# Performance work log

Hardware: AMD Instinct MI355X
Metric: run time of the kernel (lower is better)

The kernel has to match this reference:

```python
import math
import jax
import jax.numpy as jnp
import numpy as np

GRID = 12  # distance + 1 for distance-11 surface code


def _ln(x, s, b):
    m = jnp.mean(x, axis=-1, keepdims=True)
    v = jnp.mean((x - m) ** 2, axis=-1, keepdims=True)
    return (x - m) / jnp.sqrt(v + 1e-5) * s + b


def _gelu(x):
    return jax.nn.gelu(x, approximate=False)  # torch F.gelu default = exact erf


def _forward(meas, event, leak, event_leak, bias, pm_w, pm_b, pe_w, pe_b, pl_w, pl_b, pel_w, pel_b,
             stab_emb, cyc_emb, er_ln_s, er_ln_b, er_fc1_w, er_fc1_b, er_fc2_w, er_fc2_b,
             ln1_s, ln1_b, Wb, Wq, bq, Wk, bk, Wv, bv, Wo, bo, ln2_s, ln2_b,
             f1_w, f1_b, f2_w, f2_b, conv_w, conv_b, lnf_s, lnf_b,
             P, sc_w, sc_b, dr_w, dr_b, rb1_w, rb1_b, rb2_w, rb2_b, out_w, out_b,
             stab_ids, cycle_ids):
    B, T, S = meas.shape
    L, Hh, _, da = Wq.shape
    dm = Wv.shape[-1]
    d = P.shape[0]

    # per-head additive attention bias, identical across cycles: (L,B,H,S,S)
    Bp = jnp.einsum('bijd,ldh->lbhij', bias, Wb)
    scale = 1.0 / jnp.sqrt(jnp.asarray(da, meas.dtype))
    pos_emb = stab_emb[stab_ids]  # (S, d)

    def embed(t):
        h = (meas[:, t, :, None] * pm_w + pm_b
             + event[:, t, :, None] * pe_w + pe_b
             + leak[:, t, :, None] * pl_w + pl_b
             + event_leak[:, t, :, None] * pel_w + pel_b
             + pos_emb[None] + cyc_emb[cycle_ids[t]][None, None, :])
        for r in range(er_fc1_w.shape[0]):
            hn = _ln(h, er_ln_s[r], er_ln_b[r])
            h = h + jnp.matmul(_gelu(jnp.matmul(hn, er_fc1_w[r]) + er_fc1_b[r]), er_fc2_w[r]) + er_fc2_b[r]
        return h

    X = jnp.zeros((B, S, d), meas.dtype)
    for t in range(T):  # recurrent application of RNNCore over cycles
        X = (X + embed(t)) / jnp.sqrt(jnp.asarray(2.0, meas.dtype))
        for l in range(L):
            Xn = _ln(X, ln1_s[l], ln1_b[l])
            Q = jnp.einsum('bsd,hde->bhse', Xn, Wq[l]) + bq[l][None, :, None, :]
            Kt = jnp.einsum('bsd,hde->bhse', Xn, Wk[l]) + bk[l][None, :, None, :]
            V = jnp.einsum('bsd,hdm->bhsm', Xn, Wv[l]) + bv[l][None, :, None, :]
            Sc = jnp.einsum('bhqe,bhke->bhqk', Q, Kt) + Bp[l]  # bias added BEFORE 1/sqrt(da)
            A = jax.nn.softmax(Sc * scale, axis=-1)
            O = jnp.einsum('bhqk,bhkm->bhqm', A, V)
            Y = O.transpose(0, 2, 1, 3).reshape(B, S, Hh * dm)
            X = X + jnp.matmul(Y, Wo[l]) + bo[l]
            Xn = _ln(X, ln2_s[l], ln2_b[l])
            Yf = jnp.matmul(Xn, f1_w[l]) + f1_b[l]
            a, g = jnp.split(Yf, 2, axis=-1)
            X = X + jnp.matmul(_gelu(a) * g, f2_w[l]) + f2_b[l]
            # conv block: residual depth-mixing Conv1d(k=3, SAME) over the stabilizer axis
            xc = jnp.transpose(X, (0, 2, 1))  # (B, d, S)
            c = jax.lax.conv_general_dilated(xc, conv_w[l], (1,), 'SAME',
                                             dimension_numbers=('NCH', 'OIH', 'NCH'))
            X = X + _gelu(jnp.transpose(c + conv_b[l][None, :, None], (0, 2, 1)))

    # readout
    Xn = _ln(X, lnf_s, lnf_b)
    pad = jnp.broadcast_to(P, (B, GRID * GRID - S, d))  # empty grid cells filled with P
    grid = jnp.concatenate([Xn, pad], axis=1).reshape(B, GRID, GRID, d).transpose(0, 3, 1, 2)
    x = jax.lax.conv_general_dilated(grid, sc_w, (2, 2), 'VALID',
                                     dimension_numbers=('NCHW', 'OIHW', 'NCHW')) + sc_b[None, :, None, None]
    x = _gelu(x)
    x = jnp.einsum('bdhw,rd->brhw', x, dr_w) + dr_b[None, :, None, None]
    x = _gelu(x)
    x = x.mean(axis=2)  # basis 'z': pool over grid rows -> (B, rd, K)
    Kk = x.shape[2]
    x = x.transpose(0, 2, 1).reshape(B * Kk, -1)
    for r in range(rb1_w.shape[0]):
        x = x + jnp.matmul(_gelu(jnp.matmul(x, rb1_w[r]) + rb1_b[r]), rb2_w[r]) + rb2_b[r]
    logits = (jnp.matmul(x, out_w) + out_b).reshape(B, Kk).mean(axis=1)
    return logits


def setup_inputs() -> dict:
    key = jax.random.key(0)
    ks = iter(jax.random.split(key, 100))

    def rn(shape, s=0.02):
        return (s * jax.random.normal(next(ks), shape)).astype(jnp.float32)

    B, T, S, d = 16, 8, 120, 128
    L, H, da, dm, db = 2, 4, 32, 32, 32
    rd, nrb, ncyc = 48, 16, 32
    z = lambda *sh: jnp.zeros(sh, jnp.float32)
    o = lambda *sh: jnp.ones(sh, jnp.float32)
    inp = {
        'meas': jax.random.uniform(next(ks), (B, T, S), jnp.float32),
        'event': jax.random.uniform(next(ks), (B, T, S), jnp.float32),
        'leak': jax.random.uniform(next(ks), (B, T, S), jnp.float32),
        'event_leak': jax.random.uniform(next(ks), (B, T, S), jnp.float32),
        'bias': rn((B, S, S, db), 0.5),
        'pm_w': rn((d,)), 'pm_b': z(d),
        'pe_w': rn((d,)), 'pe_b': z(d),
        'pl_w': rn((d,)), 'pl_b': z(d),
        'pel_w': rn((d,)), 'pel_b': z(d),
        'stab_emb': rn((S, d)),
        'cyc_emb': rn((ncyc, d)),
        'er_ln_s': o(2, d), 'er_ln_b': z(2, d),
        'er_fc1_w': rn((2, d, d)), 'er_fc1_b': z(2, d),
        'er_fc2_w': rn((2, d, d)), 'er_fc2_b': z(2, d),
        'ln1_s': o(L, d), 'ln1_b': z(L, d),
        'Wb': rn((L, db, H)),
        'Wq': rn((L, H, d, da)), 'bq': z(L, H, da),
        'Wk': rn((L, H, d, da)), 'bk': z(L, H, da),
        'Wv': rn((L, H, d, dm)), 'bv': z(L, H, dm),
        'Wo': rn((L, H * dm, d)), 'bo': z(L, d),
        'ln2_s': o(L, d), 'ln2_b': z(L, d),
        'f1_w': rn((L, d, 4 * d)), 'f1_b': z(L, 4 * d),
        'f2_w': rn((L, 2 * d, d)), 'f2_b': z(L, d),
        'conv_w': rn((L, d, d, 3)), 'conv_b': z(L, d),
        'lnf_s': o(d), 'lnf_b': z(d),
        'P': z(d),
        'sc_w': rn((d, d, 2, 2)), 'sc_b': z(d),
        'dr_w': rn((rd, d)), 'dr_b': z(rd),
        'rb1_w': rn((nrb, rd, rd)), 'rb1_b': z(nrb, rd),
        'rb2_w': rn((nrb, rd, rd)), 'rb2_b': z(nrb, rd),
        'out_w': rn((rd,)), 'out_b': z(),
        'stab_ids': jnp.arange(S, dtype=jnp.int32),
        'cycle_ids': jnp.arange(T, dtype=jnp.int32),
    }
    return inp


def reference(meas, event, leak, event_leak, bias, pm_w, pm_b, pe_w, pe_b, pl_w, pl_b, pel_w, pel_b,
              stab_emb, cyc_emb, er_ln_s, er_ln_b, er_fc1_w, er_fc1_b, er_fc2_w, er_fc2_b,
              ln1_s, ln1_b, Wb, Wq, bq, Wk, bk, Wv, bv, Wo, bo, ln2_s, ln2_b,
              f1_w, f1_b, f2_w, f2_b, conv_w, conv_b, lnf_s, lnf_b,
              P, sc_w, sc_b, dr_w, dr_b, rb1_w, rb1_b, rb2_w, rb2_b, out_w, out_b,
              stab_ids, cycle_ids):
    return _forward(meas, event, leak, event_leak, bias, pm_w, pm_b, pe_w, pe_b, pl_w, pl_b, pel_w, pel_b,
                    stab_emb, cyc_emb, er_ln_s, er_ln_b, er_fc1_w, er_fc1_b, er_fc2_w, er_fc2_b,
                    ln1_s, ln1_b, Wb, Wq, bq, Wk, bk, Wv, bv, Wo, bo, ln2_s, ln2_b,
                    f1_w, f1_b, f2_w, f2_b, conv_w, conv_b, lnf_s, lnf_b,
                    P, sc_w, sc_b, dr_w, dr_b, rb1_w, rb1_b, rb2_w, rb2_b, out_w, out_b,
                    stab_ids, cycle_ids)
```

## Files before the change

kernel.cpp:

```cpp
#include <hip/hip_runtime.h>
#include <math.h>

#define Dm 128
#define Ssz 120
#define Bsz 16
#define Tcy 8
#define Hh 4
#define DA 32
#define Lly 2
#define RT 8
#define NRT ((Bsz*Ssz)/RT)
#define NROW (Bsz*Ssz)

struct KParams {
    const float *meas, *event_, *leak, *event_leak, *bias;
    const float *pm_w, *pm_b, *pe_w, *pe_b, *pl_w, *pl_b, *pel_w, *pel_b;
    const float *stab_emb, *cyc_emb;
    const float *er_ln_s, *er_ln_b, *er_fc1_w, *er_fc1_b, *er_fc2_w, *er_fc2_b;
    const float *ln1_s, *ln1_b, *Wb, *Wq, *bq, *Wk, *bk, *Wv, *bv, *Wo, *bo;
    const float *ln2_s, *ln2_b, *f1_w, *f1_b, *f2_w, *f2_b, *conv_w, *conv_b;
    const float *lnf_s, *lnf_b, *Pp, *sc_w, *sc_b, *dr_w, *dr_b;
    const float *rb1_w, *rb1_b, *rb2_w, *rb2_b, *out_w, *out_b;
    const int *stab_ids, *cycle_ids;
    float *Bp, *Q, *K, *V, *Y2, *cwT, *E;
};

__device__ __forceinline__ float gelu_f(float x) {
    return 0.5f * x * (1.0f + erff(x * 0.70710678118654752f));
}

__device__ __forceinline__ int swz16(int i, int per_b) {
    return ((((i & 7) << 1) | ((i >> 3) & 1)) * per_b) + (i >> 4);
}

__device__ __forceinline__ void ln_rows8(const float (*src)[Dm], float (*dst)[Dm],
                                         const float* sg, const float* bg, int tid) {
    int r = tid >> 6, g = tid & 63;
    float x0 = src[r][g], x1 = src[r][g + 64];
    float s1 = x0 + x1;
#pragma unroll
    for (int off = 32; off; off >>= 1) s1 += __shfl_xor(s1, off);
    float m = s1 * (1.f / 128.f);
    float d0 = x0 - m, d1 = x1 - m;
    float s2 = d0 * d0 + d1 * d1;
#pragma unroll
    for (int off = 32; off; off >>= 1) s2 += __shfl_xor(s2, off);
    float rstd = rsqrtf(s2 * (1.f / 128.f) + 1e-5f);
    dst[r][g]      = d0 * rstd * sg[g]      + bg[g];
    dst[r][g + 64] = d1 * rstd * sg[g + 64] + bg[g + 64];
}

__device__ __forceinline__ void ln32(const float (*src)[Dm], float (*dst)[Dm],
                                     const float* sg, const float* bg, int tid) {
    int r = tid >> 4, g = tid & 15;
    float v[8];
    float s1 = 0.f;
#pragma unroll
    for (int k = 0; k < 8; k++) { v[k] = src[r][g + 16 * k]; s1 += v[k]; }
#pragma unroll
    for (int off = 8; off; off >>= 1) s1 += __shfl_xor(s1, off);
    float m = s1 * (1.f / 128.f);
    float s2 = 0.f;
#pragma unroll
    for (int k = 0; k < 8; k++) { float d = v[k] - m; s2 += d * d; }
#pragma unroll
    for (int off = 8; off; off >>= 1) s2 += __shfl_xor(s2, off);
    float rstd = rsqrtf(s2 * (1.f / 128.f) + 1e-5f);
#pragma unroll
    for (int k = 0; k < 8; k++)
        dst[r][g + 16 * k] = (v[k] - m) * rstd * sg[g + 16 * k] + bg[g + 16 * k];
}

__global__ __launch_bounds__(256) void k_prepcw(KParams p) {
    int idx = blockIdx.x * 256 + threadIdx.x;
    if (idx >= Lly * Dm * 3 * Dm) return;
    int o = idx & 127; int rest = idx >> 7;
    int k = rest % 3; rest /= 3;
    int i = rest & 127; int l = rest >> 7;
    p.cwT[idx] = p.conv_w[((l * Dm + o) * Dm + i) * 3 + k];
}

__global__ __launch_bounds__(128) void k_bias(KParams p) {
    int blk = blockIdx.x;
    int b = blk / Ssz, i = blk % Ssz;
    int j = threadIdx.x;
    if (j >= Ssz) return;
    const float4* br4 = (const float4*)(p.bias + ((size_t)(b * Ssz + i) * Ssz + j) * 32);
    float a[Lly][4];
#pragma unroll
    for (int l = 0; l < Lly; l++)
#pragma unroll
        for (int h = 0; h < 4; h++) a[l][h] = 0.f;
#pragma unroll
    for (int c4 = 0; c4 < 8; c4++) {
        float bv[4]; *(float4*)bv = br4[c4];
#pragma unroll
        for (int u = 0; u < 4; u++) {
#pragma unroll
            for (int l = 0; l < Lly; l++) {
                const float* w = p.Wb + (l * 32 + c4 * 4 + u) * Hh;
                a[l][0] += bv[u] * w[0]; a[l][1] += bv[u] * w[1];
                a[l][2] += bv[u] * w[2]; a[l][3] += bv[u] * w[3];
            }
        }
    }
    size_t hs = (size_t)Ssz * Ssz;
#pragma unroll
    for (int l = 0; l < Lly; l++) {
        size_t base = (((size_t)(l * Bsz + b) * Hh) * Ssz + i) * Ssz + j;
        p.Bp[base] = a[l][0]; p.Bp[base + hs] = a[l][1];
        p.Bp[base + 2 * hs] = a[l][2]; p.Bp[base + 3 * hs] = a[l][3];
    }
}

__global__ __launch_bounds__(512) void k_embed_all(KParams p) {
    __shared__ float h[32][Dm], hn[32][Dm], t1[32][Dm];
    int t = blockIdx.x / 60, tile = blockIdx.x % 60;
    int row0 = tile * 32;
    int tid = threadIdx.x;
    int cid = p.cycle_ids[t];
    for (int idx = tid; idx < 32 * Dm; idx += 512) {
        int r = idx >> 7, j = idx & 127;
        int row = row0 + r;
        int b = row / Ssz, s = row % Ssz;
        int sid = p.stab_ids[s];
        int mi = (b * Tcy + t) * Ssz + s;
        h[r][j] = p.meas[mi] * p.pm_w[j] + p.pm_b[j]
                + p.event_[mi] * p.pe_w[j] + p.pe_b[j]
                + p.leak[mi] * p.pl_w[j] + p.pl_b[j]
                + p.event_leak[mi] * p.pel_w[j] + p.pel_b[j]
                + p.stab_emb[sid * Dm + j] + p.cyc_emb[cid * Dm + j];
    }
    __syncthreads();
    int g2 = tid >> 7, j = tid & 127;
    for (int rbk = 0; rbk < 2; rbk++) {
        ln32(h, hn, p.er_ln_s + rbk * Dm, p.er_ln_b + rbk * Dm, tid);
        __syncthreads();
        const float* W1 = p.er_fc1_w + rbk * Dm * Dm;
        float acc[8];
#pragma unroll
        for (int rr = 0; rr < 8; rr++) acc[rr] = 0.f;
#pragma unroll 2
        for (int i4 = 0; i4 < 32; i4++) {
            float4 xv[8];
#pragma unroll
            for (int rr = 0; rr < 8; rr++) xv[rr] = *(const float4*)&hn[8 * g2 + rr][i4 * 4];
#pragma unroll
            for (int u = 0; u < 4; u++) {
                float w = W1[(i4 * 4 + u) * Dm + j];
#pragma unroll
                for (int rr = 0; rr < 8; rr++) acc[rr] += ((const float*)&xv[rr])[u] * w;
            }
        }
        float b1 = p.er_fc1_b[rbk * Dm + j];
#pragma unroll
        for (int rr = 0; rr < 8; rr++) t1[8 * g2 + rr][j] = gelu_f(acc[rr] + b1);
        __syncthreads();
        const float* W2 = p.er_fc2_w + rbk * Dm * Dm;
#pragma unroll
        for (int rr = 0; rr < 8; rr++) acc[rr] = 0.f;
#pragma unroll 2
        for (int i4 = 0; i4 < 32; i4++) {
            float4 xv[8];
#pragma unroll
            for (int rr = 0; rr < 8; rr++) xv[rr] = *(const float4*)&t1[8 * g2 + rr][i4 * 4];
#pragma unroll
            for (int u = 0; u < 4; u++) {
                float w = W2[(i4 * 4 + u) * Dm + j];
#pragma unroll
                for (int rr = 0; rr < 8; rr++) acc[rr] += ((const float*)&xv[rr])[u] * w;
            }
        }
        float b2 = p.er_fc2_b[rbk * Dm + j];
#pragma unroll
        for (int rr = 0; rr < 8; rr++) h[8 * g2 + rr][j] += acc[rr] + b2;
        __syncthreads();
    }
    for (int idx = tid; idx < 32 * Dm; idx += 512) {
        int r = idx >> 7, jj = idx & 127;
        p.E[((size_t)t * NROW + row0 + r) * Dm + jj] = h[r][jj];
    }
}

__global__ __launch_bounds__(512) void k_a(KParams p, const float* Xprev, float* Xcur,
                                           int l, int t, int doConv) {
    __shared__ float xr[RT + 2][Dm];
    __shared__ float xn[RT][Dm];
    int rb = swz16(blockIdx.x, Ssz / RT);
    int row0 = rb * RT;
    int b = row0 / Ssz, s0 = row0 % Ssz;
    int tid = threadIdx.x;
    const float inv = 0.70710678118654752f;
    int g2 = tid >> 7, j = tid & 127;

    if (doConv) {
        int lconv = l ^ 1;
        {
            float4* xr4 = (float4*)&xr[0][0];
            for (int i = tid; i < (RT + 2) * Dm / 4; i += 512) {
                int rr = i >> 5, c = i & 31;
                int s = s0 + rr - 1;
                float4 v = make_float4(0.f, 0.f, 0.f, 0.f);
                if (s >= 0 && s < Ssz) v = *(const float4*)(Xprev + (b * Ssz + s) * Dm + 4 * c);
                xr4[i] = v;
            }
        }
        __syncthreads();
        const float* CW = p.cwT + (size_t)lconv * Dm * 3 * Dm + j;
        float a0 = 0.f, a1 = 0.f;
#pragma unroll 2
        for (int i4 = 0; i4 < 32; i4++) {
            float4 xv[4];
#pragma unroll
            for (int rr = 0; rr < 4; rr++) xv[rr] = *(const float4*)&xr[2 * g2 + rr][i4 * 4];
#pragma unroll
            for (int u = 0; u < 4; u++) {
                int i = i4 * 4 + u;
                float w0 = CW[(i * 3 + 0) * Dm];
                float w1 = CW[(i * 3 + 1) * Dm];
                float w2 = CW[(i * 3 + 2) * Dm];
                a0 += w0 * ((const float*)&xv[0])[u] + w1 * ((const float*)&xv[1])[u] + w2 * ((const float*)&xv[2])[u];
                a1 += w0 * ((const float*)&xv[1])[u] + w1 * ((const float*)&xv[2])[u] + w2 * ((const float*)&xv[3])[u];
            }
        }
        float cb = p.conv_b[lconv * Dm + j];
        float v0 = xr[2 * g2 + 1][j] + gelu_f(a0 + cb);
        float v1 = xr[2 * g2 + 2][j] + gelu_f(a1 + cb);
        if (l == 0) {
            v0 = (v0 + p.E[((size_t)t * NROW + row0 + 2 * g2) * Dm + j]) * inv;
            v1 = (v1 + p.E[((size_t)t * NROW + row0 + 2 * g2 + 1) * Dm + j]) * inv;
        }
        Xcur[(row0 + 2 * g2) * Dm + j]     = v0;
        Xcur[(row0 + 2 * g2 + 1) * Dm + j] = v1;
        xn[2 * g2][j] = v0; xn[2 * g2 + 1][j] = v1;
    } else {
        float v0 = p.E[(size_t)(row0 + 2 * g2) * Dm + j] * inv;
        float v1 = p.E[(size_t)(row0 + 2 * g2 + 1) * Dm + j] * inv;
        Xcur[(row0 + 2 * g2) * Dm + j]     = v0;
        Xcur[(row0 + 2 * g2 + 1) * Dm + j] = v1;
        xn[2 * g2][j] = v0; xn[2 * g2 + 1][j] = v1;
    }
    __syncthreads();
    ln_rows8(xn, xn, p.ln1_s + l * Dm, p.ln1_b + l * Dm, tid);
    __syncthreads();
    if (tid < 384) {
        int out = tid >> 7, col = tid & 127;
        int h = col >> 5, e = col & 31;
        const float* W = (out == 0 ? p.Wq : out == 1 ? p.Wk : p.Wv)
                       + ((size_t)(l * Hh + h) * Dm) * DA + e;
        const float* bbp = (out == 0 ? p.bq : out == 1 ? p.bk : p.bv) + (l * Hh + h) * DA + e;
        float acc[8];
#pragma unroll
        for (int rr = 0; rr < 8; rr++) acc[rr] = 0.f;
#pragma unroll 2
        for (int i4 = 0; i4 < 32; i4++) {
            float4 xv[8];
#pragma unroll
            for (int rr = 0; rr < 8; rr++) xv[rr] = *(const float4*)&xn[rr][i4 * 4];
#pragma unroll
            for (int u = 0; u < 4; u++) {
                float w = W[(i4 * 4 + u) * DA];
#pragma unroll
                for (int rr = 0; rr < 8; rr++) acc[rr] += ((const float*)&xv[rr])[u] * w;
            }
        }
        float bv = bbp[0];
        if (out == 2) {
            float* vb = p.V + ((size_t)(b * Hh + h) * DA + e) * Ssz + s0;
            *(float4*)vb       = make_float4(acc[0] + bv, acc[1] + bv, acc[2] + bv, acc[3] + bv);
            *(float4*)(vb + 4) = make_float4(acc[4] + bv, acc[5] + bv, acc[6] + bv, acc[7] + bv);
        } else {
            float* dst = (out == 0 ? p.Q : p.K);
            size_t base = ((size_t)(b * Hh + h) * Ssz + s0) * DA + e;
#pragma unroll
            for (int rr = 0; rr < 8; rr++) dst[base + rr * DA] = acc[rr] + bv;
        }
    }
}

__global__ __launch_bounds__(512) void k_b(KParams p, float* X, int l) {
    __shared__ float4 Kh4[Ssz][8];
    __shared__ float4 Vt4[DA][32];
    __shared__ float sc[RT][Ssz];
    __shared__ float dn[RT];
    __shared__ float Yt[RT][Dm];
    __shared__ float pvp[2][RT][DA];
    __shared__ float opW[2][RT][Dm];
    __shared__ float xres[RT][Dm];
    __shared__ float xn[RT][Dm];
    __shared__ float yfg[RT][256];
    __shared__ float yg[RT][256];
    int rb = swz16(blockIdx.x, Ssz / RT);
    int b = rb / (Ssz / RT), qt = rb % (Ssz / RT);
    int q0 = qt * RT;
    int row0 = rb * RT;
    int tid = threadIdx.x;
    const float scale = 0.17677669529663689f;

    for (int h = 0; h < Hh; h++) {
        __syncthreads();
        {
            const float4* K4 = (const float4*)(p.K + ((size_t)(b * Hh + h) * Ssz) * DA);
            const float4* V4 = (const float4*)(p.V + ((size_t)(b * Hh + h) * DA) * Ssz);
            for (int i = tid; i < 960; i += 512) {
                int k = i >> 3, f = i & 7;
                Kh4[k][f ^ (k & 7)] = K4[i];
                int e = i / 30, s4 = i % 30;
                Vt4[e][s4 ^ (e & 7)] = V4[i];
            }
        }
        __syncthreads();
        {
            int r = tid >> 6, c0 = tid & 63;
            int c1 = c0 + 64;
            bool v1 = c1 < Ssz;
            int sw = c0 & 7;
            const float* Bpr = p.Bp + (((size_t)(l * Bsz + b) * Hh + h) * Ssz + q0 + r) * Ssz;
            const float4* Q4r = (const float4*)(p.Q + ((size_t)(b * Hh + h) * Ssz + q0 + r) * DA);
            float d0 = 0.f, d1 = 0.f;
#pragma unroll
            for (int e4 = 0; e4 < 8; e4++) {
                float4 qv = Q4r[e4];
                float4 k0 = Kh4[c0][e4 ^ sw];
                d0 += qv.x * k0.x + qv.y * k0.y + qv.z * k0.z + qv.w * k0.w;
                if (v1) {
                    float4 k1 = Kh4[c1][e4 ^ sw];
                    d1 += qv.x * k1.x + qv.y * k1.y + qv.z * k1.z + qv.w * k1.w;
                }
            }
            d0 = (d0 + Bpr[c0]) * scale;
            d1 = v1 ? (d1 + Bpr[c1]) * scale : -1e30f;
            float m = fmaxf(d0, d1);
#pragma unroll
            for (int off = 32; off; off >>= 1) m = fmaxf(m, __shfl_xor(m, off));
            float p0 = expf(d0 - m);
            float p1 = v1 ? expf(d1 - m) : 0.f;
            float s = p0 + p1;
#pragma unroll
            for (int off = 32; off; off >>= 1) s += __shfl_xor(s, off);
            sc[r][c0] = p0;
            if (v1) sc[r][c1] = p1;
            if (c0 == 0) dn[r] = s;
        }
        __syncthreads();
        {
            int half = tid >> 8, r = (tid >> 5) & 7, m = tid & 31;
            int sw = m & 7;
            int k40 = half * 15;
            float a = 0.f;
#pragma unroll
            for (int k4 = 0; k4 < 15; k4++) {
                float s4v[4];
                *(float4*)s4v = *(const float4*)&sc[r][(k40 + k4) * 4];
                float4 vv = Vt4[m][(k40 + k4) ^ sw];
                a += s4v[0] * vv.x + s4v[1] * vv.y + s4v[2] * vv.z + s4v[3] * vv.w;
            }
            pvp[half][r][m] = a;
        }
        __syncthreads();
        if (tid < 256) {
            int r = tid >> 5, m = tid & 31;
            Yt[r][h * DA + m] = (pvp[0][r][m] + pvp[1][r][m]) / dn[r];
        }
    }
    __syncthreads();
    {
        int pp = tid >> 8, g2 = (tid >> 7) & 1, j = tid & 127;
        {
            const float* W = p.Wo + l * Dm * Dm + j;
            float a[4] = {0.f, 0.f, 0.f, 0.f};
            for (int k4 = pp * 16; k4 < pp * 16 + 16; k4++) {
                float4 yv[4];
#pragma unroll
                for (int rr = 0; rr < 4; rr++) yv[rr] = *(const float4*)&Yt[4 * g2 + rr][k4 * 4];
#pragma unroll
                for (int u = 0; u < 4; u++) {
                    float w = W[(k4 * 4 + u) * Dm];
#pragma unroll
                    for (int rr = 0; rr < 4; rr++) a[rr] += ((const float*)&yv[rr])[u] * w;
                }
            }
#pragma unroll
            for (int rr = 0; rr < 4; rr++) opW[pp][4 * g2 + rr][j] = a[rr];
        }
        __syncthreads();
        for (int idx = tid; idx < RT * Dm; idx += 512) {
            int r = idx >> 7, j2 = idx & 127;
            float xv = X[(row0 + r) * Dm + j2] + opW[0][r][j2] + opW[1][r][j2] + p.bo[l * Dm + j2];
            xres[r][j2] = xv;
            xn[r][j2] = xv;
        }
        __syncthreads();
        ln_rows8(xn, xn, p.ln2_s + l * Dm, p.ln2_b + l * Dm, tid);
        __syncthreads();
        {
            const float* W1 = p.f1_w + (size_t)l * Dm * 512 + tid;
            float acc[8];
#pragma unroll
            for (int rr = 0; rr < 8; rr++) acc[rr] = 0.f;
#pragma unroll 2
            for (int i4 = 0; i4 < 32; i4++) {
                float4 xv[8];
#pragma unroll
                for (int rr = 0; rr < 8; rr++) xv[rr] = *(const float4*)&xn[rr][i4 * 4];
#pragma unroll
                for (int u = 0; u < 4; u++) {
                    float w = W1[(i4 * 4 + u) * 512];
#pragma unroll
                    for (int rr = 0; rr < 8; rr++) acc[rr] += ((const float*)&xv[rr])[u] * w;
                }
            }
            if (tid >= 256) {
#pragma unroll
                for (int rr = 0; rr < 8; rr++) yfg[rr][tid - 256] = acc[rr];
            }
            __syncthreads();
            if (tid < 256) {
                float b1a = p.f1_b[l * 512 + tid];
                float b1g = p.f1_b[l * 512 + 256 + tid];
#pragma unroll
                for (int rr = 0; rr < 8; rr++)
                    yg[rr][tid] = gelu_f(acc[rr] + b1a) * (yfg[rr][tid] + b1g);
            }
        }
        __syncthreads();
        {
            const float* W2 = p.f2_w + (size_t)l * 256 * Dm + j;
            float a[4] = {0.f, 0.f, 0.f, 0.f};
            for (int k4 = pp * 32; k4 < pp * 32 + 32; k4++) {
                float4 yv[4];
#pragma unroll
                for (int rr = 0; rr < 4; rr++) yv[rr] = *(const float4*)&yg[4 * g2 + rr][k4 * 4];
#pragma unroll
                for (int u = 0; u < 4; u++) {
                    float w = W2[(k4 * 4 + u) * Dm];
#pragma unroll
                    for (int rr = 0; rr < 4; rr++) a[rr] += ((const float*)&yv[rr])[u] * w;
                }
            }
#pragma unroll
            for (int rr = 0; rr < 4; rr++) opW[pp][4 * g2 + rr][j] = a[rr];
        }
        __syncthreads();
        for (int idx = tid; idx < RT * Dm; idx += 512) {
            int r = idx >> 7, j2 = idx & 127;
            X[(row0 + r) * Dm + j2] = xres[r][j2] + opW[0][r][j2] + opW[1][r][j2] + p.f2_b[l * Dm + j2];
        }
    }
}

__global__ __launch_bounds__(256) void k_conv(KParams p, const float* Xin, float* Xout, int l) {
    __shared__ float xr[RT + 2][Dm];
    int rb = swz16(blockIdx.x, Ssz / RT);
    int row0 = rb * RT;
    int b = row0 / Ssz, s0 = row0 % Ssz;
    int tid = threadIdx.x;
    {
        float4* xr4 = (float4*)&xr[0][0];
        for (int i = tid; i < (RT + 2) * Dm / 4; i += 256) {
            int rr = i >> 5, c = i & 31;
            int s = s0 + rr - 1;
            float4 v = make_float4(0.f, 0.f, 0.f, 0.f);
            if (s >= 0 && s < Ssz) v = *(const float4*)(Xin + (b * Ssz + s) * Dm + 4 * c);
            xr4[i] = v;
        }
    }
    __syncthreads();
    int g = tid >> 7, j = tid & 127;
    const float* CW = p.cwT + (size_t)l * Dm * 3 * Dm + j;
    float a[4] = {0.f, 0.f, 0.f, 0.f};
#pragma unroll 2
    for (int i4 = 0; i4 < 32; i4++) {
        float4 xv[6];
#pragma unroll
        for (int rr = 0; rr < 6; rr++) xv[rr] = *(const float4*)&xr[4 * g + rr][i4 * 4];
#pragma unroll
        for (int u = 0; u < 4; u++) {
            int i = i4 * 4 + u;
            float w0 = CW[(i * 3 + 0) * Dm];
            float w1 = CW[(i * 3 + 1) * Dm];
            float w2 = CW[(i * 3 + 2) * Dm];
#pragma unroll
            for (int rr = 0; rr < 4; rr++)
                a[rr] += w0 * ((const float*)&xv[rr])[u]
                       + w1 * ((const float*)&xv[rr + 1])[u]
                       + w2 * ((const float*)&xv[rr + 2])[u];
        }
    }
    float cb = p.conv_b[l * Dm + j];
#pragma unroll
    for (int rr = 0; rr < 4; rr++)
        Xout[(row0 + 4 * g + rr) * Dm + j] = xr[4 * g + rr + 1][j] + gelu_f(a[rr] + cb);
}

__global__ __launch_bounds__(128) void k_head(KParams p, const float* X) {
    int blk = swz16(blockIdx.x, 36);
    int b = blk / 36, r2 = blk % 36, oh = r2 / 6, ow = r2 % 6;
    __shared__ float cells[4][Dm];
    __shared__ float sx[Dm];
    int tid = threadIdx.x;
    {
        int c = tid >> 5, lane = tid & 31;
        int cell = (2 * oh + (c >> 1)) * 12 + (2 * ow + (c & 1));
        if (cell < Ssz) {
            const float* Xr = X + (size_t)(b * Ssz + cell) * Dm;
            float v[4];
            float s1 = 0.f;
#pragma unroll
            for (int k = 0; k < 4; k++) { v[k] = Xr[lane + 32 * k]; s1 += v[k]; }
#pragma unroll
            for (int off = 16; off; off >>= 1) s1 += __shfl_xor(s1, off);
            float m = s1 * (1.f / 128.f);
            float s2 = 0.f;
#pragma unroll
            for (int k = 0; k < 4; k++) { float d = v[k] - m; s2 += d * d; }
#pragma unroll
            for (int off = 16; off; off >>= 1) s2 += __shfl_xor(s2, off);
            float rstd = rsqrtf(s2 * (1.f / 128.f) + 1e-5f);
#pragma unroll
            for (int k = 0; k < 4; k++) {
                int jj = lane + 32 * k;
                cells[c][jj] = (v[k] - m) * rstd * p.lnf_s[jj] + p.lnf_b[jj];
            }
        } else {
#pragma unroll
            for (int k = 0; k < 4; k++) cells[c][lane + 32 * k] = p.Pp[lane + 32 * k];
        }
    }
    __syncthreads();
    int j = tid;
    float acc = p.sc_b[j];
    const float* W = p.sc_w + (size_t)j * Dm * 4;
    for (int i = 0; i < Dm; i++) {
        acc += W[i * 4 + 0] * cells[0][i] + W[i * 4 + 1] * cells[1][i]
             + W[i * 4 + 2] * cells[2][i] + W[i * 4 + 3] * cells[3][i];
    }
    sx[j] = gelu_f(acc);
    __syncthreads();
    if (j < 48) {
        float a = p.dr_b[j];
        const float* w = p.dr_w + j * Dm;
        for (int i = 0; i < Dm; i++) a += sx[i] * w[i];
        p.Y2[((b * 6 + ow) * 6 + oh) * 48 + j] = gelu_f(a);
    }
}

__global__ __launch_bounds__(320) void k_rb2(KParams p, float* out) {
    int b = swz16(blockIdx.x, 1);
    __shared__ float x[6][48], t[6][48], red[6];
    int tid = threadIdx.x;
    int ow = tid / 48, j = tid % 48;
    bool act = tid < 288;
    if (act) {
        float s = 0.f;
#pragma unroll
        for (int oh = 0; oh < 6; oh++) s += p.Y2[((b * 6 + ow) * 6 + oh) * 48 + j];
        x[ow][j] = s * (1.f / 6.f);
    }
    __syncthreads();
    for (int r = 0; r < 16; r++) {
        if (act) {
            float a = p.rb1_b[r * 48 + j];
            const float* W = p.rb1_w + (size_t)r * 48 * 48 + j;
            for (int i = 0; i < 48; i++) a += x[ow][i] * W[i * 48];
            t[ow][j] = gelu_f(a);
        }
        __syncthreads();
        if (act) {
            float a = p.rb2_b[r * 48 + j];
            const float* W = p.rb2_w + (size_t)r * 48 * 48 + j;
            for (int i = 0; i < 48; i++) a += t[ow][i] * W[i * 48];
            x[ow][j] += a;
        }
        __syncthreads();
    }
    if (act) t[ow][j] = x[ow][j] * p.out_w[j];
    __syncthreads();
    if (tid < 6) {
        float s = 0.f;
        for (int i = 0; i < 48; i++) s += t[tid][i];
        red[tid] = s;
    }
    __syncthreads();
    if (tid == 0) {
        float s = 0.f;
#pragma unroll
        for (int w = 0; w < 6; w++) s += red[w];
        out[b] = s * (1.f / 6.f) + p.out_b[0];
    }
}

extern "C" void kernel_launch(void* const* d_in, const int* in_sizes, int n_in,
                              void* d_out, int out_size, void* d_ws, size_t ws_size,
                              hipStream_t stream) {
    KParams p;
    p.meas       = (const float*)d_in[0];
    p.event_     = (const float*)d_in[1];
    p.leak       = (const float*)d_in[2];
    p.event_leak = (const float*)d_in[3];
    p.bias       = (const float*)d_in[4];
    p.pm_w  = (const float*)d_in[5];  p.pm_b  = (const float*)d_in[6];
    p.pe_w  = (const float*)d_in[7];  p.pe_b  = (const float*)d_in[8];
    p.pl_w  = (const float*)d_in[9];  p.pl_b  = (const float*)d_in[10];
    p.pel_w = (const float*)d_in[11]; p.pel_b = (const float*)d_in[12];
    p.stab_emb = (const float*)d_in[13];
    p.cyc_emb  = (const float*)d_in[14];
    p.er_ln_s  = (const float*)d_in[15]; p.er_ln_b  = (const float*)d_in[16];
    p.er_fc1_w = (const float*)d_in[17]; p.er_fc1_b = (const float*)d_in[18];
    p.er_fc2_w = (const float*)d_in[19]; p.er_fc2_b = (const float*)d_in[20];
    p.ln1_s = (const float*)d_in[21]; p.ln1_b = (const float*)d_in[22];
    p.Wb = (const float*)d_in[23];
    p.Wq = (const float*)d_in[24]; p.bq = (const float*)d_in[25];
    p.Wk = (const float*)d_in[26]; p.bk = (const float*)d_in[27];
    p.Wv = (const float*)d_in[28]; p.bv = (const float*)d_in[29];
    p.Wo = (const float*)d_in[30]; p.bo = (const float*)d_in[31];
    p.ln2_s = (const float*)d_in[32]; p.ln2_b = (const float*)d_in[33];
    p.f1_w = (const float*)d_in[34]; p.f1_b = (const float*)d_in[35];
    p.f2_w = (const float*)d_in[36]; p.f2_b = (const float*)d_in[37];
    p.conv_w = (const float*)d_in[38]; p.conv_b = (const float*)d_in[39];
    p.lnf_s = (const float*)d_in[40]; p.lnf_b = (const float*)d_in[41];
    p.Pp   = (const float*)d_in[42];
    p.sc_w = (const float*)d_in[43]; p.sc_b = (const float*)d_in[44];
    p.dr_w = (const float*)d_in[45]; p.dr_b = (const float*)d_in[46];
    p.rb1_w = (const float*)d_in[47]; p.rb1_b = (const float*)d_in[48];
    p.rb2_w = (const float*)d_in[49]; p.rb2_b = (const float*)d_in[50];
    p.out_w = (const float*)d_in[51]; p.out_b = (const float*)d_in[52];
    p.stab_ids  = (const int*)d_in[53];
    p.cycle_ids = (const int*)d_in[54];

    float* ws = (float*)d_ws;
    size_t off = 0;
    const size_t BP_SZ  = (size_t)Lly * Bsz * Hh * Ssz * Ssz;
    const size_t QKV_SZ = (size_t)Bsz * Hh * Ssz * DA;
    const size_t X_SZ   = (size_t)Bsz * Ssz * Dm;
    const size_t E_SZ   = (size_t)Tcy * NROW * Dm;
    p.Bp = ws + off; off += BP_SZ;
    p.Q  = ws + off; off += QKV_SZ;
    p.K  = ws + off; off += QKV_SZ;
    p.V  = ws + off; off += QKV_SZ;
    float* X0 = ws + off; off += X_SZ;
    float* X1 = ws + off; off += X_SZ;
    p.Y2  = ws + off; off += (size_t)Bsz * 6 * 6 * 48;
    p.cwT = ws + off; off += (size_t)Lly * Dm * 3 * Dm;
    p.E   = ws + off; off += E_SZ;

    k_prepcw<<<(Lly * Dm * 3 * Dm + 255) / 256, 256, 0, stream>>>(p);
    k_bias<<<Bsz * Ssz, 128, 0, stream>>>(p);
    k_embed_all<<<Tcy * 60, 512, 0, stream>>>(p);

    float* Xbuf[2] = {X0, X1};
    for (int step = 0; step < Tcy * Lly; step++) {
        int t = step >> 1, l = step & 1;
        float* Xcur = Xbuf[step & 1];
        const float* Xprev = (step == 0) ? X0 : Xbuf[(step + 1) & 1];
        k_a<<<NRT, 512, 0, stream>>>(p, Xprev, Xcur, l, t, step > 0 ? 1 : 0);
        k_b<<<NRT, 512, 0, stream>>>(p, Xcur, l);
    }
    k_conv<<<NRT, 256, 0, stream>>>(p, X1, X0, 1);
    k_head<<<Bsz * 36, 128, 0, stream>>>(p, X0);
    k_rb2<<<Bsz, 320, 0, stream>>>(p, (float*)d_out);
}
```

Before: 826.7 us.

## Pretranspose all weights for float4 row loads and union k_b shared buffers

A prep kernel now transposes the QKV, Wo, FFN, embed-resblock and conv weights into one workspace so that each output column's weights sit contiguously. Every matmul loop then reads its weights as float4 and accumulates with dot products, instead of issuing one strided scalar load per input element. In k_b, the attention and FFN shared-memory buffers are overlaid in a union and the launch bound asks for 6 blocks per CU, aiming to raise occupancy. The cost is one extra transpose pass each call. The per-thread float4 loads are no longer coalesced across threads, since neighbouring threads now read rows 512 bytes apart.

After: 1.730 ms. 109% more time.

```diff
diff --git a/kernel.cpp b/kernel.cpp
--- a/kernel.cpp
+++ b/kernel.cpp
@@ -12,6 +12,15 @@
 #define NRT ((Bsz*Ssz)/RT)
 #define NROW (Bsz*Ssz)
 
+#define WT_QKV 0
+#define WT_WO  98304
+#define WT_F1  131072
+#define WT_F2  262144
+#define WT_E1  327680
+#define WT_E2  360448
+#define WT_CW  393216
+#define WT_TOT 491520
+
 struct KParams {
     const float *meas, *event_, *leak, *event_leak, *bias;
     const float *pm_w, *pm_b, *pe_w, *pe_b, *pl_w, *pl_b, *pel_w, *pel_b;
@@ -22,11 +31,14 @@
     const float *lnf_s, *lnf_b, *Pp, *sc_w, *sc_b, *dr_w, *dr_b;
     const float *rb1_w, *rb1_b, *rb2_w, *rb2_b, *out_w, *out_b;
     const int *stab_ids, *cycle_ids;
-    float *Bp, *Q, *K, *V, *Y2, *cwT, *E;
+    float *Bp, *Q, *K, *V, *Y2, *E, *wT;
 };
 
 __device__ __forceinline__ float gelu_f(float x) {
     return 0.5f * x * (1.0f + erff(x * 0.70710678118654752f));
+}
+__device__ __forceinline__ float dot4(float4 a, float4 b) {
+    return a.x * b.x + a.y * b.y + a.z * b.z + a.w * b.w;
 }
 
 __device__ __forceinline__ int swz16(int i, int per_b) {
@@ -71,13 +83,50 @@
         dst[r][g + 16 * k] = (v[k] - m) * rstd * sg[g + 16 * k] + bg[g + 16 * k];
 }
 
-__global__ __launch_bounds__(256) void k_prepcw(KParams p) {
+__global__ __launch_bounds__(256) void k_prepw(KParams p) {
     int idx = blockIdx.x * 256 + threadIdx.x;
-    if (idx >= Lly * Dm * 3 * Dm) return;
-    int o = idx & 127; int rest = idx >> 7;
-    int k = rest % 3; rest /= 3;
-    int i = rest & 127; int l = rest >> 7;
-    p.cwT[idx] = p.conv_w[((l * Dm + o) * Dm + i) * 3 + k];
+    if (idx >= WT_TOT) return;
+    float v;
+    if (idx < WT_WO) {
+        int i = idx & 127; int t = idx >> 7;
+        int hcol = t & 127; t >>= 7;
+        int l = t & 1; int out = t >> 1;
+        int h = hcol >> 5, e = hcol & 31;
+        const float* W = (out == 0 ? p.Wq : out == 1 ? p.Wk : p.Wv);
+        v = W[(((size_t)(l * Hh + h) * Dm) + i) * DA + e];
+    } else if (idx < WT_F1) {
+        int rel = idx - WT_WO;
+        int k = rel & 127; int t = rel >> 7;
+        int j = t & 127; int l = t >> 7;
+        v = p.Wo[(size_t)l * Dm * Dm + k * Dm + j];
+    } else if (idx < WT_F2) {
+        int rel = idx - WT_F1;
+        int i = rel & 127; int t = rel >> 7;
+        int c = t & 511; int l = t >> 9;
+        v = p.f1_w[(size_t)l * Dm * 512 + i * 512 + c];
+    } else if (idx < WT_E1) {
+        int rel = idx - WT_F2;
+        int k = rel & 255; int t = rel >> 8;
+        int j = t & 127; int l = t >> 7;
+        v = p.f2_w[(size_t)l * 256 * Dm + k * Dm + j];
+    } else if (idx < WT_E2) {
+        int rel = idx - WT_E1;
+        int i = rel & 127; int t = rel >> 7;
+        int j = t & 127; int rbk = t >> 7;
+        v = p.er_fc1_w[(size_t)rbk * Dm * Dm + i * Dm + j];
+    } else if (idx < WT_CW) {
+        int rel = idx - WT_E2;
+        int i = rel & 127; int t = rel >> 7;
+        int j = t & 127; int rbk = t >> 7;
+        v = p.er_fc2_w[(size_t)rbk * Dm * Dm + i * Dm + j];
+    } else {
+        int rel = idx - WT_CW;
+        int i = rel & 127; int t = rel >> 7;
+        int k = t % 3; t /= 3;
+        int o = t & 127; int l = t >> 7;
+        v = p.conv_w[(((size_t)l * Dm + o) * Dm + i) * 3 + k];
+    }
+    p.wT[idx] = v;
 }
 
 __global__ __launch_bounds__(128) void k_bias(KParams p) {
@@ -136,40 +185,30 @@
     for (int rbk = 0; rbk < 2; rbk++) {
         ln32(h, hn, p.er_ln_s + rbk * Dm, p.er_ln_b + rbk * Dm, tid);
         __syncthreads();
-        const float* W1 = p.er_fc1_w + rbk * Dm * Dm;
+        const float* W1c = p.wT + WT_E1 + (((size_t)rbk * Dm + j) << 7);
         float acc[8];
 #pragma unroll
         for (int rr = 0; rr < 8; rr++) acc[rr] = 0.f;
 #pragma unroll 2
         for (int i4 = 0; i4 < 32; i4++) {
-            float4 xv[8];
-#pragma unroll
-            for (int rr = 0; rr < 8; rr++) xv[rr] = *(const float4*)&hn[8 * g2 + rr][i4 * 4];
-#pragma unroll
-            for (int u = 0; u < 4; u++) {
-                float w = W1[(i4 * 4 + u) * Dm + j];
-#pragma unroll
-                for (int rr = 0; rr < 8; rr++) acc[rr] += ((const float*)&xv[rr])[u] * w;
-            }
+            float4 w4 = *(const float4*)&W1c[i4 * 4];
+#pragma unroll
+            for (int rr = 0; rr < 8; rr++)
+                acc[rr] += dot4(*(const float4*)&hn[8 * g2 + rr][i4 * 4], w4);
         }
         float b1 = p.er_fc1_b[rbk * Dm + j];
 #pragma unroll
         for (int rr = 0; rr < 8; rr++) t1[8 * g2 + rr][j] = gelu_f(acc[rr] + b1);
         __syncthreads();
-        const float* W2 = p.er_fc2_w + rbk * Dm * Dm;
+        const float* W2c = p.wT + WT_E2 + (((size_t)rbk * Dm + j) << 7);
 #pragma unroll
         for (int rr = 0; rr < 8; rr++) acc[rr] = 0.f;
 #pragma unroll 2
         for (int i4 = 0; i4 < 32; i4++) {
-            float4 xv[8];
-#pragma unroll
-            for (int rr = 0; rr < 8; rr++) xv[rr] = *(const float4*)&t1[8 * g2 + rr][i4 * 4];
-#pragma unroll
-            for (int u = 0; u < 4; u++) {
-                float w = W2[(i4 * 4 + u) * Dm + j];
-#pragma unroll
-                for (int rr = 0; rr < 8; rr++) acc[rr] += ((const float*)&xv[rr])[u] * w;
-            }
+            float4 w4 = *(const float4*)&W2c[i4 * 4];
+#pragma unroll
+            for (int rr = 0; rr < 8; rr++)
+                acc[rr] += dot4(*(const float4*)&t1[8 * g2 + rr][i4 * 4], w4);
         }
         float b2 = p.er_fc2_b[rbk * Dm + j];
 #pragma unroll
@@ -206,22 +245,19 @@
             }
         }
         __syncthreads();
-        const float* CW = p.cwT + (size_t)lconv * Dm * 3 * Dm + j;
+        const float* CW = p.wT + WT_CW + ((((size_t)lconv * Dm + j) * 3) << 7);
         float a0 = 0.f, a1 = 0.f;
 #pragma unroll 2
         for (int i4 = 0; i4 < 32; i4++) {
-            float4 xv[4];
-#pragma unroll
-            for (int rr = 0; rr < 4; rr++) xv[rr] = *(const float4*)&xr[2 * g2 + rr][i4 * 4];
-#pragma unroll
-            for (int u = 0; u < 4; u++) {
-                int i = i4 * 4 + u;
-                float w0 = CW[(i * 3 + 0) * Dm];
-                float w1 = CW[(i * 3 + 1) * Dm];
-                float w2 = CW[(i * 3 + 2) * Dm];
-                a0 += w0 * ((const float*)&xv[0])[u] + w1 * ((const float*)&xv[1])[u] + w2 * ((const float*)&xv[2])[u];
-                a1 += w0 * ((const float*)&xv[1])[u] + w1 * ((const float*)&xv[2])[u] + w2 * ((const float*)&xv[3])[u];
-            }
+            float4 w0 = *(const float4*)&CW[i4 * 4];
+            float4 w1 = *(const float4*)&CW[128 + i4 * 4];
+            float4 w2 = *(const float4*)&CW[256 + i4 * 4];
+            float4 x0 = *(const float4*)&xr[2 * g2][i4 * 4];
+            float4 x1 = *(const float4*)&xr[2 * g2 + 1][i4 * 4];
+            float4 x2 = *(const float4*)&xr[2 * g2 + 2][i4 * 4];
+            float4 x3 = *(const float4*)&xr[2 * g2 + 3][i4 * 4];
+            a0 += dot4(w0, x0) + dot4(w1, x1) + dot4(w2, x2);
+            a1 += dot4(w0, x1) + dot4(w1, x2) + dot4(w2, x3);
         }
         float cb = p.conv_b[lconv * Dm + j];
         float v0 = xr[2 * g2 + 1][j] + gelu_f(a0 + cb);
@@ -246,23 +282,17 @@
     if (tid < 384) {
         int out = tid >> 7, col = tid & 127;
         int h = col >> 5, e = col & 31;
-        const float* W = (out == 0 ? p.Wq : out == 1 ? p.Wk : p.Wv)
-                       + ((size_t)(l * Hh + h) * Dm) * DA + e;
+        const float* Wc = p.wT + WT_QKV + (((size_t)(out * Lly + l) * Dm + col) << 7);
         const float* bbp = (out == 0 ? p.bq : out == 1 ? p.bk : p.bv) + (l * Hh + h) * DA + e;
         float acc[8];
 #pragma unroll
         for (int rr = 0; rr < 8; rr++) acc[rr] = 0.f;
 #pragma unroll 2
         for (int i4 = 0; i4 < 32; i4++) {
-            float4 xv[8];
-#pragma unroll
-            for (int rr = 0; rr < 8; rr++) xv[rr] = *(const float4*)&xn[rr][i4 * 4];
-#pragma unroll
-            for (int u = 0; u < 4; u++) {
-                float w = W[(i4 * 4 + u) * DA];
-#pragma unroll
-                for (int rr = 0; rr < 8; rr++) acc[rr] += ((const float*)&xv[rr])[u] * w;
-            }
+            float4 w4 = *(const float4*)&Wc[i4 * 4];
+#pragma unroll
+            for (int rr = 0; rr < 8; rr++)
+                acc[rr] += dot4(*(const float4*)&xn[rr][i4 * 4], w4);
         }
         float bv = bbp[0];
         if (out == 2) {
@@ -278,18 +308,24 @@
     }
 }
 
-__global__ __launch_bounds__(512) void k_b(KParams p, float* X, int l) {
-    __shared__ float4 Kh4[Ssz][8];
-    __shared__ float4 Vt4[DA][32];
-    __shared__ float sc[RT][Ssz];
+struct AttnBufs {
+    float4 Kh4[Ssz][8];
+    float4 Vt4[DA][32];
+    float sc[RT][Ssz];
+    float pvp[2][RT][DA];
+};
+struct FfnBufs {
+    float opW[2][RT][Dm];
+    float xres[RT][Dm];
+    float xn[RT][Dm];
+    float yfg[RT][256];
+    float yg[RT][256];
+};
+
+__global__ __launch_bounds__(512, 6) void k_b(KParams p, float* X, int l) {
+    __shared__ union UB { AttnBufs a; FfnBufs f; } u;
+    __shared__ float Yt[RT][Dm];
     __shared__ float dn[RT];
-    __shared__ float Yt[RT][Dm];
-    __shared__ float pvp[2][RT][DA];
-    __shared__ float opW[2][RT][Dm];
-    __shared__ float xres[RT][Dm];
-    __shared__ float xn[RT][Dm];
-    __shared__ float yfg[RT][256];
-    __shared__ float yg[RT][256];
     int rb = swz16(blockIdx.x, Ssz / RT);
     int b = rb / (Ssz / RT), qt = rb % (Ssz / RT);
     int q0 = qt * RT;
@@ -304,9 +340,9 @@
             const float4* V4 = (const float4*)(p.V + ((size_t)(b * Hh + h) * DA) * Ssz);
             for (int i = tid; i < 960; i += 512) {
                 int k = i >> 3, f = i & 7;
-                Kh4[k][f ^ (k & 7)] = K4[i];
+                u.a.Kh4[k][f ^ (k & 7)] = K4[i];
                 int e = i / 30, s4 = i % 30;
-                Vt4[e][s4 ^ (e & 7)] = V4[i];
+                u.a.Vt4[e][s4 ^ (e & 7)] = V4[i];
             }
         }
         __syncthreads();
@@ -321,12 +357,9 @@
 #pragma unroll
             for (int e4 = 0; e4 < 8; e4++) {
                 float4 qv = Q4r[e4];
-                float4 k0 = Kh4[c0][e4 ^ sw];
-                d0 += qv.x * k0.x + qv.y * k0.y + qv.z * k0.z + qv.w * k0.w;
-                if (v1) {
-                    float4 k1 = Kh4[c1][e4 ^ sw];
-                    d1 += qv.x * k1.x + qv.y * k1.y + qv.z * k1.z + qv.w * k1.w;
-                }
+                float4 k0 = u.a.Kh4[c0][e4 ^ sw];
+                d0 += dot4(qv, k0);
+                if (v1) d1 += dot4(qv, u.a.Kh4[c1][e4 ^ sw]);
             }
             d0 = (d0 + Bpr[c0]) * scale;
             d1 = v1 ? (d1 + Bpr[c1]) * scale : -1e30f;
@@ -338,8 +371,8 @@
             float s = p0 + p1;
 #pragma unroll
             for (int off = 32; off; off >>= 1) s += __shfl_xor(s, off);
-            sc[r][c0] = p0;
-            if (v1) sc[r][c1] = p1;
+            u.a.sc[r][c0] = p0;
+            if (v1) u.a.sc[r][c1] = p1;
             if (c0 == 0) dn[r] = s;
         }
         __syncthreads();
@@ -350,69 +383,58 @@
             float a = 0.f;
 #pragma unroll
             for (int k4 = 0; k4 < 15; k4++) {
-                float s4v[4];
-                *(float4*)s4v = *(const float4*)&sc[r][(k40 + k4) * 4];
-                float4 vv = Vt4[m][(k40 + k4) ^ sw];
-                a += s4v[0] * vv.x + s4v[1] * vv.y + s4v[2] * vv.z + s4v[3] * vv.w;
-            }
-            pvp[half][r][m] = a;
+                float4 s4v = *(const float4*)&u.a.sc[r][(k40 + k4) * 4];
+                float4 vv = u.a.Vt4[m][(k40 + k4) ^ sw];
+                a += dot4(s4v, vv);
+            }
+            u.a.pvp[half][r][m] = a;
         }
         __syncthreads();
         if (tid < 256) {
             int r = tid >> 5, m = tid & 31;
-            Yt[r][h * DA + m] = (pvp[0][r][m] + pvp[1][r][m]) / dn[r];
+            Yt[r][h * DA + m] = (u.a.pvp[0][r][m] + u.a.pvp[1][r][m]) / dn[r];
         }
     }
     __syncthreads();
     {
         int pp = tid >> 8, g2 = (tid >> 7) & 1, j = tid & 127;
         {
-            const float* W = p.Wo + l * Dm * Dm + j;
+            const float* Wc = p.wT + WT_WO + (((size_t)l * Dm + j) << 7);
             float a[4] = {0.f, 0.f, 0.f, 0.f};
             for (int k4 = pp * 16; k4 < pp * 16 + 16; k4++) {
-                float4 yv[4];
-#pragma unroll
-                for (int rr = 0; rr < 4; rr++) yv[rr] = *(const float4*)&Yt[4 * g2 + rr][k4 * 4];
-#pragma unroll
-                for (int u = 0; u < 4; u++) {
-                    float w = W[(k4 * 4 + u) * Dm];
-#pragma unroll
-                    for (int rr = 0; rr < 4; rr++) a[rr] += ((const float*)&yv[rr])[u] * w;
-                }
-            }
-#pragma unroll
-            for (int rr = 0; rr < 4; rr++) opW[pp][4 * g2 + rr][j] = a[rr];
+                float4 w4 = *(const float4*)&Wc[k4 * 4];
+#pragma unroll
+                for (int rr = 0; rr < 4; rr++)
+                    a[rr] += dot4(*(const float4*)&Yt[4 * g2 + rr][k4 * 4], w4);
+            }
+#pragma unroll
+            for (int rr = 0; rr < 4; rr++) u.f.opW[pp][4 * g2 + rr][j] = a[rr];
         }
         __syncthreads();
         for (int idx = tid; idx < RT * Dm; idx += 512) {
             int r = idx >> 7, j2 = idx & 127;
-            float xv = X[(row0 + r) * Dm + j2] + opW[0][r][j2] + opW[1][r][j2] + p.bo[l * Dm + j2];
-            xres[r][j2] = xv;
-            xn[r][j2] = xv;
-        }
-        __syncthreads();
-        ln_rows8(xn, xn, p.ln2_s + l * Dm, p.ln2_b + l * Dm, tid);
+            float xv = X[(row0 + r) * Dm + j2] + u.f.opW[0][r][j2] + u.f.opW[1][r][j2] + p.bo[l * Dm + j2];
+            u.f.xres[r][j2] = xv;
+            u.f.xn[r][j2] = xv;
+        }
+        __syncthreads();
+        ln_rows8(u.f.xn, u.f.xn, p.ln2_s + l * Dm, p.ln2_b + l * Dm, tid);
         __syncthreads();
         {
-            const float* W1 = p.f1_w + (size_t)l * Dm * 512 + tid;
+            const float* Wc = p.wT + WT_F1 + (((size_t)l * 512 + tid) << 7);
             float acc[8];
 #pragma unroll
             for (int rr = 0; rr < 8; rr++) acc[rr] = 0.f;
 #pragma unroll 2
             for (int i4 = 0; i4 < 32; i4++) {
-                float4 xv[8];
-#pragma unroll
-                for (int rr = 0; rr < 8; rr++) xv[rr] = *(const float4*)&xn[rr][i4 * 4];
-#pragma unroll
-                for (int u = 0; u < 4; u++) {
-                    float w = W1[(i4 * 4 + u) * 512];
-#pragma unroll
-                    for (int rr = 0; rr < 8; rr++) acc[rr] += ((const float*)&xv[rr])[u] * w;
-                }
+                float4 w4 = *(const float4*)&Wc[i4 * 4];
+#pragma unroll
+                for (int rr = 0; rr < 8; rr++)
+                    acc[rr] += dot4(*(const float4*)&u.f.xn[rr][i4 * 4], w4);
             }
             if (tid >= 256) {
 #pragma unroll
-                for (int rr = 0; rr < 8; rr++) yfg[rr][tid - 256] = acc[rr];
+                for (int rr = 0; rr < 8; rr++) u.f.yfg[rr][tid - 256] = acc[rr];
             }
             __syncthreads();
             if (tid < 256) {
@@ -420,31 +442,26 @@
                 float b1g = p.f1_b[l * 512 + 256 + tid];
 #pragma unroll
                 for (int rr = 0; rr < 8; rr++)
-                    yg[rr][tid] = gelu_f(acc[rr] + b1a) * (yfg[rr][tid] + b1g);
+                    u.f.yg[rr][tid] = gelu_f(acc[rr] + b1a) * (u.f.yfg[rr][tid] + b1g);
             }
         }
         __syncthreads();
         {
-            const float* W2 = p.f2_w + (size_t)l * 256 * Dm + j;
+            const float* Wc = p.wT + WT_F2 + (((size_t)l * Dm + j) << 8);
             float a[4] = {0.f, 0.f, 0.f, 0.f};
             for (int k4 = pp * 32; k4 < pp * 32 + 32; k4++) {
-                float4 yv[4];
-#pragma unroll
-                for (int rr = 0; rr < 4; rr++) yv[rr] = *(const float4*)&yg[4 * g2 + rr][k4 * 4];
-#pragma unroll
-                for (int u = 0; u < 4; u++) {
-                    float w = W2[(k4 * 4 + u) * Dm];
-#pragma unroll
-                    for (int rr = 0; rr < 4; rr++) a[rr] += ((const float*)&yv[rr])[u] * w;
-                }
-            }
-#pragma unroll
-            for (int rr = 0; rr < 4; rr++) opW[pp][4 * g2 + rr][j] = a[rr];
+                float4 w4 = *(const float4*)&Wc[k4 * 4];
+#pragma unroll
+                for (int rr = 0; rr < 4; rr++)
+                    a[rr] += dot4(*(const float4*)&u.f.yg[4 * g2 + rr][k4 * 4], w4);
+            }
+#pragma unroll
+            for (int rr = 0; rr < 4; rr++) u.f.opW[pp][4 * g2 + rr][j] = a[rr];
         }
         __syncthreads();
         for (int idx = tid; idx < RT * Dm; idx += 512) {
             int r = idx >> 7, j2 = idx & 127;
-            X[(row0 + r) * Dm + j2] = xres[r][j2] + opW[0][r][j2] + opW[1][r][j2] + p.f2_b[l * Dm + j2];
+            X[(row0 + r) * Dm + j2] = u.f.xres[r][j2] + u.f.opW[0][r][j2] + u.f.opW[1][r][j2] + p.f2_b[l * Dm + j2];
         }
     }
 }
@@ -467,25 +484,19 @@
     }
     __syncthreads();
     int g = tid >> 7, j = tid & 127;
-    const float* CW = p.cwT + (size_t)l * Dm * 3 * Dm + j;
+    const float* CW = p.wT + WT_CW + ((((size_t)l * Dm + j) * 3) << 7);
     float a[4] = {0.f, 0.f, 0.f, 0.f};
 #pragma unroll 2
     for (int i4 = 0; i4 < 32; i4++) {
+        float4 w0 = *(const float4*)&CW[i4 * 4];
+        float4 w1 = *(const float4*)&CW[128 + i4 * 4];
+        float4 w2 = *(const float4*)&CW[256 + i4 * 4];
         float4 xv[6];
 #pragma unroll
         for (int rr = 0; rr < 6; rr++) xv[rr] = *(const float4*)&xr[4 * g + rr][i4 * 4];
 #pragma unroll
-        for (int u = 0; u < 4; u++) {
-            int i = i4 * 4 + u;
-            float w0 = CW[(i * 3 + 0) * Dm];
-            float w1 = CW[(i * 3 + 1) * Dm];
-            float w2 = CW[(i * 3 + 2) * Dm];
-#pragma unroll
-            for (int rr = 0; rr < 4; rr++)
-                a[rr] += w0 * ((const float*)&xv[rr])[u]
-                       + w1 * ((const float*)&xv[rr + 1])[u]
-                       + w2 * ((const float*)&xv[rr + 2])[u];
-        }
+        for (int rr = 0; rr < 4; rr++)
+            a[rr] += dot4(w0, xv[rr]) + dot4(w1, xv[rr + 1]) + dot4(w2, xv[rr + 2]);
     }
     float cb = p.conv_b[l * Dm + j];
 #pragma unroll
@@ -641,10 +652,10 @@
     float* X0 = ws + off; off += X_SZ;
     float* X1 = ws + off; off += X_SZ;
     p.Y2  = ws + off; off += (size_t)Bsz * 6 * 6 * 48;
-    p.cwT = ws + off; off += (size_t)Lly * Dm * 3 * Dm;
     p.E   = ws + off; off += E_SZ;
-
-    k_prepcw<<<(Lly * Dm * 3 * Dm + 255) / 256, 256, 0, stream>>>(p);
+    p.wT  = ws + off; off += WT_TOT;
+
+    k_prepw<<<(WT_TOT + 255) / 256, 256, 0, stream>>>(p);
     k_bias<<<Bsz * Ssz, 128, 0, stream>>>(p);
     k_embed_all<<<Tcy * 60, 512, 0, stream>>>(p);
 
```
